# Performance work log

Measured on AMD Instinct MI355X. Metric: run time of the kernel, lower is better.

Reference implementation:

```python
import jax, jax.numpy as jnp
import numpy as np

N, E, IN, H, C, L = 50000, 800000, 256, 128, 50, 3
EPS = 1e-5  # BatchNorm1d eps


def setup_inputs() -> dict:
    key = jax.random.key(0)
    ks = jax.random.split(key, 16)
    s = 0.05  # weight init scale
    return dict(
        features=jax.random.normal(ks[0], (N, IN), jnp.float32),
        src=jax.random.randint(ks[1], (E,), 0, N, jnp.int32),
        dst=jax.random.randint(ks[2], (E,), 0, N, jnp.int32),
        w_in=jax.random.normal(ks[3], (IN, H), jnp.float32) * s,
        b_in=jnp.zeros((H,), jnp.float32),
        gc_w=jax.random.normal(ks[4], (L, H, H), jnp.float32) * s,
        gc_b=jnp.zeros((L, H), jnp.float32),
        bn_gamma=jnp.ones((L, H), jnp.float32),
        bn_beta=jnp.zeros((L, H), jnp.float32),
        bn_mean=jax.random.normal(ks[5], (L, H), jnp.float32) * 0.1,
        bn_var=jax.random.uniform(ks[6], (L, H), jnp.float32, 0.5, 1.5),
        attn_w1=jax.random.normal(ks[7], (2 * H, H), jnp.float32) * s,
        attn_b1=jnp.zeros((H,), jnp.float32),
        attn_w2=jax.random.normal(ks[8], (H, 1), jnp.float32) * s,
        attn_b2=jnp.zeros((1,), jnp.float32),
        agg_w=jax.random.normal(ks[9], (2 * H, H), jnp.float32) * s,
        agg_b=jnp.zeros((H,), jnp.float32),
        out_w=jax.random.normal(ks[10], (H, C), jnp.float32) * s,
        out_b=jnp.zeros((C,), jnp.float32),
    )


def reference(features, src, dst, w_in, b_in, gc_w, gc_b, bn_gamma, bn_beta,
              bn_mean, bn_var, attn_w1, attn_b1, attn_w2, attn_b2,
              agg_w, agg_b, out_w, out_b):
    seg = lambda v, i: jax.ops.segment_sum(v, i, num_segments=N)
    ones_e = jnp.ones((E,), features.dtype)
    in_deg = seg(ones_e, dst)    # [N] in-degree (dst side)
    out_deg = seg(ones_e, src)   # [N] out-degree (src side)

    # input_encoder (dropout = identity at inference)
    h = jax.nn.relu(features @ w_in + b_in)  # [N, H]

    # aggregate_neighbor_types: copy_u + mean (0 for zero in-degree)
    neigh = seg(h[src], dst) / jnp.maximum(in_deg, 1.0)[:, None]
    agg = jax.nn.relu(jnp.concatenate([h, neigh], axis=1) @ agg_w + agg_b)

    # relation attention: MLP -> sigmoid gate, gated residual add
    a = jax.nn.relu(jnp.concatenate([h, agg], axis=1) @ attn_w1 + attn_b1)
    attn = jax.nn.sigmoid(a @ attn_w2 + attn_b2)  # [N, 1]
    h_att = h + agg * attn

    # DGL GraphConv norm='both', clamp(min=1), aggregate-then-matmul
    inv_out = jnp.maximum(out_deg, 1.0)[:, None] ** -0.5
    inv_in = jnp.maximum(in_deg, 1.0)[:, None] ** -0.5
    for i in range(L):
        x = h_att if i == 0 else h
        rst = seg((x * inv_out)[src], dst) * inv_in  # normalized SpMM
        rst = rst @ gc_w[i] + gc_b[i]
        # BatchNorm1d (eval: running stats)
        rst = (rst - bn_mean[i]) * (bn_gamma[i] * jax.lax.rsqrt(bn_var[i] + EPS)) + bn_beta[i]
        rst = jax.nn.relu(rst)
        if i > 0:
            rst = rst + h  # residual
        h = rst

    return h @ out_w + out_b  # [N, C]
```

## Files before the change

### kernel.cpp

```cpp
#include <hip/hip_runtime.h>
#include <hip/hip_fp16.h>
#include <math.h>

constexpr int NN  = 50000;
constexpr int EE  = 800000;
constexpr int INF_ = 256;
constexpr int HF  = 128;
constexpr int CC  = 50;
constexpr long NH = (long)NN * HF;
constexpr int NSL = 32;
constexpr int ESL = EE / NSL;
constexpr int CHK = 12500;
#define EPSV 1e-5f

enum { EPI_RELU = 0, EPI_NONE = 1, EPI_BN = 2, EPI_BN_RES = 3, EPI_ATTN = 4 };
enum { H16_NONE = 0, H16_SCALED = 2 };

typedef __attribute__((ext_vector_type(4))) float f32x4;
typedef __attribute__((ext_vector_type(8))) _Float16 f16x8;


__global__ __launch_bounds__(256) void count_partial2_kernel(
    const int4* __restrict__ dst4, const int4* __restrict__ src4,
    unsigned* __restrict__ pd, unsigned* __restrict__ ps) {
  __shared__ unsigned cnt[CHK];
  int bb = blockIdx.x;
  const int which = bb >> 7;
  bb &= 127;
  const int4* keys4 = which ? src4 : dst4;
  unsigned* partials = which ? ps : pd;
  const int chunk = bb & 3;
  const int sl = bb >> 2;
  for (int i = threadIdx.x; i < CHK; i += 256) cnt[i] = 0;
  __syncthreads();
  const int base4 = sl * (ESL / 4);
  const int lo = chunk * CHK;
  for (int i = threadIdx.x; i < ESL / 4; i += 256) {
    int4 k = keys4[base4 + i];
    int a;
    a = k.x - lo; if ((unsigned)a < (unsigned)CHK) atomicAdd(&cnt[a], 1u);
    a = k.y - lo; if ((unsigned)a < (unsigned)CHK) atomicAdd(&cnt[a], 1u);
    a = k.z - lo; if ((unsigned)a < (unsigned)CHK) atomicAdd(&cnt[a], 1u);
    a = k.w - lo; if ((unsigned)a < (unsigned)CHK) atomicAdd(&cnt[a], 1u);
  }
  __syncthreads();
  unsigned* p = partials + (long)sl * NN + lo;
  for (int i = threadIdx.x; i < CHK; i += 256) p[i] = cnt[i];
}

__global__ __launch_bounds__(256) void deg_scan_kernel(
    const unsigned* __restrict__ pd, const unsigned* __restrict__ ps,
    int* __restrict__ row_ptr, int* __restrict__ bsum,
    float* __restrict__ inv_mean, float* __restrict__ inv_in,
    float* __restrict__ inv_out) {
  __shared__ int sh[256];
  int n = blockIdx.x * 256 + threadIdx.x;
  unsigned di = 0, dz = 0;
  if (n < NN) {
    #pragma unroll 8
    for (int sl = 0; sl < NSL; ++sl) {
      di += pd[(long)sl * NN + n];
      dz += ps[(long)sl * NN + n];
    }
    float fdi = fmaxf((float)di, 1.f), fdz = fmaxf((float)dz, 1.f);
    inv_mean[n] = 1.f / fdi;
    inv_in[n]  = rsqrtf(fdi);
    inv_out[n] = rsqrtf(fdz);
  }
  int v = (n < NN) ? (int)di : 0;
  sh[threadIdx.x] = v;
  __syncthreads();
  #pragma unroll
  for (int off = 1; off < 256; off <<= 1) {
    int tv = (threadIdx.x >= off) ? sh[threadIdx.x - off] : 0;
    __syncthreads();
    sh[threadIdx.x] += tv;
    __syncthreads();
  }
  if (n < NN) row_ptr[n] = sh[threadIdx.x] - v;
  if (threadIdx.x == 255) bsum[blockIdx.x] = sh[255];
}

__global__ __launch_bounds__(256) void scan_block_kernel(const int* __restrict__ counts,
                                                         int* excl, int* bsum, int n) {
  __shared__ int sh[256];
  int i = blockIdx.x * 256 + threadIdx.x;
  int v = (i < n) ? counts[i] : 0;
  sh[threadIdx.x] = v;
  __syncthreads();
  #pragma unroll
  for (int off = 1; off < 256; off <<= 1) {
    int tv = (threadIdx.x >= off) ? sh[threadIdx.x - off] : 0;
    __syncthreads();
    sh[threadIdx.x] += tv;
    __syncthreads();
  }
  if (i < n) excl[i] = sh[threadIdx.x] - v;
  if (threadIdx.x == 255 && bsum) bsum[blockIdx.x] = sh[255];
}

__global__ void cursor_init_kernel(const int* __restrict__ row_ptr, const int* __restrict__ bsum,
                                   const unsigned* __restrict__ pd,
                                   unsigned* __restrict__ cur0,
                                   const float* __restrict__ inv_mean,
                                   const float* __restrict__ inv_in,
                                   int4* __restrict__ nodeinfo) {
  int n = blockIdx.x * 256 + threadIdx.x;
  if (n >= NN) return;
  unsigned start = (unsigned)(row_ptr[n] + bsum[n >> 8]);
  unsigned run = start;
  #pragma unroll 8
  for (int sl = 0; sl < NSL; ++sl) {
    cur0[(long)sl * NN + n] = run;
    run += pd[(long)sl * NN + n];
  }
  nodeinfo[n] = make_int4((int)start, (int)run,
                          __float_as_int(inv_mean[n]), __float_as_int(inv_in[n]));
}

__global__ __launch_bounds__(256) void fill_partial_kernel(
    const int4* __restrict__ dst4, const int4* __restrict__ src4,
    const unsigned* __restrict__ cur0, int* __restrict__ col) {
  __shared__ unsigned cur[CHK];
  const int chunk = blockIdx.x & 3;
  const int sl = blockIdx.x >> 2;
  const int lo = chunk * CHK;
  const unsigned* c0 = cur0 + (long)sl * NN + lo;
  for (int i = threadIdx.x; i < CHK; i += 256) cur[i] = c0[i];
  __syncthreads();
  const int base4 = sl * (ESL / 4);
  for (int i = threadIdx.x; i < ESL / 4; i += 256) {
    int4 d = dst4[base4 + i];
    int4 s = src4[base4 + i];
    int a;
    a = d.x - lo; if ((unsigned)a < (unsigned)CHK) col[atomicAdd(&cur[a], 1u)] = s.x;
    a = d.y - lo; if ((unsigned)a < (unsigned)CHK) col[atomicAdd(&cur[a], 1u)] = s.y;
    a = d.z - lo; if ((unsigned)a < (unsigned)CHK) col[atomicAdd(&cur[a], 1u)] = s.z;
    a = d.w - lo; if ((unsigned)a < (unsigned)CHK) col[atomicAdd(&cur[a], 1u)] = s.w;
  }
}


__global__ __launch_bounds__(256) void spmm32p_kernel(
    const int4* __restrict__ nodeinfo, const int* __restrict__ cols,
    const __half* __restrict__ xs, int useW,
    __half* __restrict__ outh) {
  const int t = threadIdx.x;
  const int lane = t & 63;
  const int wv = t >> 6;
  const int b = blockIdx.x;
  const int xcd = b & 7;
  const int slice = xcd >> 1;
  const int sub = xcd & 1;
  const int npair = lane >> 5;
  const int node = (b >> 3) * 16 + sub * 8 + wv * 2 + npair;
  const int e8 = (lane >> 2) & 7;
  const int q4 = lane & 3;
  const __half* xb = xs + (long)slice * NN * 32 + q4 * 8;
  int4 ni = nodeinfo[node];
  const int e0 = ni.x, end = ni.y;
  const float d = __int_as_float(useW ? ni.w : ni.z);
  const int deg = end - e0;
  int dmax = deg > 0 ? deg : 0;
  {
    int od = __shfl_xor(dmax, 32, 64);
    dmax = dmax > od ? dmax : od;
  }
  const int kmax = (dmax + 7) >> 3;
  const int ecl = (end - 1) > 0 ? (end - 1) : 0;
  const __half2 z2 = __float2half2_rn(0.f);
  __half2 A0 = z2, A1 = z2, A2 = z2, A3 = z2;
  __half2 B0 = z2, B1 = z2, B2 = z2, B3 = z2;
  int k = 0;
  for (; k + 2 <= kmax; k += 2) {
    int ee0 = e0 + k * 8 + e8;
    int ee1 = ee0 + 8;
    bool m0 = ee0 < end, m1 = ee1 < end;
    int s0 = cols[m0 ? ee0 : ecl];
    int s1 = cols[m1 ? ee1 : ecl];
    f32x4 v0 = *(const f32x4*)(xb + (unsigned)s0 * 32u);
    f32x4 v1 = *(const f32x4*)(xb + (unsigned)s1 * 32u);
    const __half2* h0 = (const __half2*)&v0;
    const __half2* h1 = (const __half2*)&v1;
    A0 = __hadd2(A0, m0 ? h0[0] : z2); A1 = __hadd2(A1, m0 ? h0[1] : z2);
    A2 = __hadd2(A2, m0 ? h0[2] : z2); A3 = __hadd2(A3, m0 ? h0[3] : z2);
    B0 = __hadd2(B0, m1 ? h1[0] : z2); B1 = __hadd2(B1, m1 ? h1[1] : z2);
    B2 = __hadd2(B2, m1 ? h1[2] : z2); B3 = __hadd2(B3, m1 ? h1[3] : z2);
  }
  if (k < kmax) {
    int ee = e0 + k * 8 + e8;
    bool m = ee < end;
    int s = cols[m ? ee : ecl];
    f32x4 v = *(const f32x4*)(xb + (unsigned)s * 32u);
    const __half2* h = (const __half2*)&v;
    A0 = __hadd2(A0, m ? h[0] : z2); A1 = __hadd2(A1, m ? h[1] : z2);
    A2 = __hadd2(A2, m ? h[2] : z2); A3 = __hadd2(A3, m ? h[3] : z2);
  }
  A0 = __hadd2(A0, B0); A1 = __hadd2(A1, B1);
  A2 = __hadd2(A2, B2); A3 = __hadd2(A3, B3);
  float2 p0 = __half22float2(A0), p1 = __half22float2(A1);
  float2 p2 = __half22float2(A2), p3 = __half22float2(A3);
  float f0 = p0.x, f1 = p0.y, f2 = p1.x, f3 = p1.y;
  float f4 = p2.x, f5 = p2.y, f6 = p3.x, f7 = p3.y;
  {
    bool hi = (lane & 4) != 0;
    float t0 = hi ? f0 : f4, t1 = hi ? f1 : f5, t2 = hi ? f2 : f6, t3 = hi ? f3 : f7;
    t0 = __shfl_xor(t0, 4, 64); t1 = __shfl_xor(t1, 4, 64);
    t2 = __shfl_xor(t2, 4, 64); t3 = __shfl_xor(t3, 4, 64);
    f0 = (hi ? f4 : f0) + t0; f1 = (hi ? f5 : f1) + t1;
    f2 = (hi ? f6 : f2) + t2; f3 = (hi ? f7 : f3) + t3;
  }
  {
    bool hi = (lane & 8) != 0;
    float t0 = hi ? f0 : f2, t1 = hi ? f1 : f3;
    t0 = __shfl_xor(t0, 8, 64); t1 = __shfl_xor(t1, 8, 64);
    f0 = (hi ? f2 : f0) + t0; f1 = (hi ? f3 : f1) + t1;
  }
  float fin;
  {
    bool hi = (lane & 16) != 0;
    float t0 = hi ? f0 : f1;
    t0 = __shfl_xor(t0, 16, 64);
    fin = (hi ? f1 : f0) + t0;
  }
  int foff = q4 * 8 + ((lane >> 2) & 1) * 4 + ((lane >> 3) & 1) * 2 + ((lane >> 4) & 1);
  outh[((long)slice * NN + node) * 32 + foff] = __float2half(fin * d);
}


constexpr int SZ256 = 8 * 8 * 512;
constexpr int SZ128 = 4 * 8 * 512;
constexpr int SZOUT = 4 * 4 * 512;
constexpr int PK_TOTAL = 3 * SZ256 + 3 * SZ128 + SZOUT;

__global__ __launch_bounds__(256) void prepack_all_kernel(
    const float* __restrict__ w_in, const float* __restrict__ agg_w,
    const float* __restrict__ at1, const float* __restrict__ gc_w,
    const float* __restrict__ out_w, ushort* __restrict__ outbase) {
  int idx = blockIdx.x * 256 + threadIdx.x;
  if (idx >= PK_TOTAL) return;
  const float* W; int N, ldw, NTpad, local; ushort* outp;
  if (idx < 3 * SZ256) {
    int s = idx / SZ256; local = idx - s * SZ256;
    W = (s == 0) ? w_in : ((s == 1) ? agg_w : at1);
    N = HF; ldw = HF; NTpad = 8;
    outp = outbase + s * SZ256;
  } else if (idx < 3 * SZ256 + 3 * SZ128) {
    int r = idx - 3 * SZ256; int s = r / SZ128; local = r - s * SZ128;
    W = gc_w + (long)s * HF * HF; N = HF; ldw = HF; NTpad = 8;
    outp = outbase + 3 * SZ256 + s * SZ128;
  } else {
    local = idx - 3 * SZ256 - 3 * SZ128;
    W = out_w; N = CC; ldw = CC; NTpad = 4;
    outp = outbase + 3 * SZ256 + 3 * SZ128;
  }
  int j    = local & 7;
  int lane = (local >> 3) & 63;
  int rest = local >> 9;
  int nt = rest % NTpad;
  int kc = rest / NTpad;
  int k = kc * 32 + (lane >> 4) * 8 + j;
  int n = nt * 16 + (lane & 15);
  float w = (n < N) ? W[(long)k * ldw + n] : 0.f;
  outp[local] = __half_as_ushort(__float2half(w));
}


template<int KC, int NT, int NTP, int EPI, int H16, int ASRC, int OUTM, int COLSPLIT, int BHOIST>
__global__ __launch_bounds__(256) void mgemm_kernel(
    const void* __restrict__ A1, int lda1,
    const void* __restrict__ A2,
    const ushort* __restrict__ Bf,
    const float* __restrict__ bias,
    const float* __restrict__ g, const float* __restrict__ be,
    const float* __restrict__ mu, const float* __restrict__ va,
    const __half* __restrict__ resp,
    float* __restrict__ outf, __half* __restrict__ outh, int ldc, int Ncols,
    __half* __restrict__ x16, const float* __restrict__ rowscale) {
  const int t = threadIdx.x;
  const int lane = t & 63;
  const int wid = t >> 6;
  const int rowbase = COLSPLIT ? (blockIdx.x * 32 + (wid >> 1) * 16)
                               : (blockIdx.x * 64 + wid * 16);
  const int colbase = COLSPLIT ? ((wid & 1) * NT * 16) : 0;
  const int arow = rowbase + (lane & 15);
  const int kgrp = (lane >> 4) * 8;
  const bool rowok = arow < NN;

  f32x4 acc[NT];
  #pragma unroll
  for (int n = 0; n < NT; ++n) acc[n] = (f32x4){0.f, 0.f, 0.f, 0.f};

  const f32x4 z4 = {0.f, 0.f, 0.f, 0.f};
  f32x4 fra[ASRC == 0 ? KC : 1], frb[ASRC == 0 ? KC : 1];
  uint4 areg[ASRC == 1 ? KC : 1];
  if (ASRC == 0) {
    #pragma unroll
    for (int kc = 0; kc < KC; ++kc) {
      const float* p = (const float*)A1 + (long)arow * lda1 + kc * 32 + kgrp;
      fra[kc] = rowok ? *(const f32x4*)p : z4;
      frb[kc] = rowok ? *(const f32x4*)(p + 4) : z4;
    }
  } else {
    #pragma unroll
    for (int kc = 0; kc < KC; ++kc) {
      const bool second = (KC == 8) && (kc >= 4);
      const ushort* At = (const ushort*)(second ? A2 : A1);
      int k0 = (second ? (kc - 4) : kc) * 32 + kgrp;
      const ushort* p = At + ((long)(k0 >> 5) * NN + arow) * 32 + (k0 & 31);
      areg[kc] = rowok ? *(const uint4*)p : make_uint4(0, 0, 0, 0);
    }
  }

  if (BHOIST) {
    uint4 breg[KC * NT];
    #pragma unroll
    for (int kc = 0; kc < KC; ++kc) {
      const ushort* bp = Bf + ((long)kc * NTP * 64 + lane) * 8 + (long)colbase * 32;
      #pragma unroll
      for (int nt = 0; nt < NT; ++nt)
        breg[kc * NT + nt] = *(const uint4*)(bp + (long)nt * 512);
    }
    #pragma unroll
    for (int kc = 0; kc < KC; ++kc) {
      union { uint4 u; f16x8 v; } cv;
      cv.u = areg[kc];
      #pragma unroll
      for (int nt = 0; nt < NT; ++nt) {
        union { uint4 u; f16x8 v; } bv;
        bv.u = breg[kc * NT + nt];
        acc[nt] = __builtin_amdgcn_mfma_f32_16x16x32_f16(cv.v, bv.v, acc[nt], 0, 0, 0);
      }
    }
  } else {
    #pragma unroll
    for (int kc = 0; kc < KC; ++kc) {
      f16x8 av;
      if (ASRC == 0) {
        #pragma unroll
        for (int j = 0; j < 4; ++j) {
          av[j]     = (_Float16)fra[kc][j];
          av[j + 4] = (_Float16)frb[kc][j];
        }
      } else {
        union { uint4 u; f16x8 v; } cv;
        cv.u = areg[kc];
        av = cv.v;
      }
      const ushort* bp = Bf + ((long)kc * NTP * 64 + lane) * 8 + (long)colbase * 32;
      #pragma unroll
      for (int nt = 0; nt < NT; ++nt) {
        union { uint4 u; f16x8 v; } bv;
        bv.u = *(const uint4*)(bp + (long)nt * 512);
        acc[nt] = __builtin_amdgcn_mfma_f32_16x16x32_f16(av, bv.v, acc[nt], 0, 0, 0);
      }
    }
  }

  const int colg = lane & 15;
  const int rsub = (lane >> 4) * 4;

  if (EPI == EPI_ATTN) {
    float part0 = 0.f, part1 = 0.f, part2 = 0.f, part3 = 0.f;
    #pragma unroll
    for (int nt = 0; nt < NT; ++nt) {
      int c = nt * 16 + colg;
      float w2v = g[c];
      float bb = bias[c];
      part0 = fmaf(fmaxf(acc[nt][0] + bb, 0.f), w2v, part0);
      part1 = fmaf(fmaxf(acc[nt][1] + bb, 0.f), w2v, part1);
      part2 = fmaf(fmaxf(acc[nt][2] + bb, 0.f), w2v, part2);
      part3 = fmaf(fmaxf(acc[nt][3] + bb, 0.f), w2v, part3);
    }
    #pragma unroll
    for (int m = 1; m <= 8; m <<= 1) {
      part0 += __shfl_xor(part0, m, 64);
      part1 += __shfl_xor(part1, m, 64);
      part2 += __shfl_xor(part2, m, 64);
      part3 += __shfl_xor(part3, m, 64);
    }
    const float b2v = be[0];
    float s0 = 1.f / (1.f + __expf(-(part0 + b2v)));
    float s1 = 1.f / (1.f + __expf(-(part1 + b2v)));
    float s2 = 1.f / (1.f + __expf(-(part2 + b2v)));
    float s3 = 1.f / (1.f + __expf(-(part3 + b2v)));
    const __half* h0t = (const __half*)A1;
    const __half* aggt = (const __half*)A2;
    #pragma unroll
    for (int nt = 0; nt < NT; ++nt) {
      int c = nt * 16 + colg;
      #pragma unroll
      for (int i = 0; i < 4; ++i) {
        int r = rowbase + rsub + i;
        if (r >= NN) continue;
        long sidx = ((long)(c >> 5) * NN + r) * 32 + (c & 31);
        float sv = (i == 0) ? s0 : ((i == 1) ? s1 : ((i == 2) ? s2 : s3));
        float h = __half2float(h0t[sidx]) + __half2float(aggt[sidx]) * sv;
        x16[sidx] = __float2half(h * rowscale[r]);
      }
    }
    return;
  }

  #pragma unroll
  for (int nt = 0; nt < NT; ++nt) {
    int c = colbase + nt * 16 + colg;
    if (c >= Ncols) continue;
    float bb = bias ? bias[c] : 0.f;
    float scale = 1.f, shift = 0.f;
    if (EPI == EPI_BN || EPI == EPI_BN_RES) {
      scale = g[c] * rsqrtf(va[c] + EPSV);
      shift = be[c] - mu[c] * scale;
    }
    #pragma unroll
    for (int i = 0; i < 4; ++i) {
      int r = rowbase + rsub + i;
      if (r >= NN) continue;
      long sidx = ((long)(c >> 5) * NN + r) * 32 + (c & 31);
      float v = acc[nt][i] + bb;
      if (EPI == EPI_RELU) {
        v = fmaxf(v, 0.f);
      } else if (EPI == EPI_BN || EPI == EPI_BN_RES) {
        v = fmaxf(v * scale + shift, 0.f);
        if (EPI == EPI_BN_RES) v += __half2float(resp[sidx]);
      }
      if (OUTM == 0) {
        outf[(long)r * ldc + c] = v;
      } else {
        outh[sidx] = __float2half(v);
        if (H16 == H16_SCALED) x16[sidx] = __float2half(v * rowscale[r]);
      }
    }
  }
}


extern "C" void kernel_launch(void* const* d_in, const int* in_sizes, int n_in,
                              void* d_out, int out_size, void* d_ws, size_t ws_size,
                              hipStream_t stream) {
  const float* features = (const float*)d_in[0];
  const int*   src      = (const int*)d_in[1];
  const int*   dst      = (const int*)d_in[2];
  const float* w_in     = (const float*)d_in[3];
  const float* b_in     = (const float*)d_in[4];
  const float* gc_w     = (const float*)d_in[5];
  const float* gc_b     = (const float*)d_in[6];
  const float* bn_gamma = (const float*)d_in[7];
  const float* bn_beta  = (const float*)d_in[8];
  const float* bn_mean  = (const float*)d_in[9];
  const float* bn_var   = (const float*)d_in[10];
  const float* attn_w1  = (const float*)d_in[11];
  const float* attn_b1  = (const float*)d_in[12];
  const float* attn_w2  = (const float*)d_in[13];
  const float* attn_b2  = (const float*)d_in[14];
  const float* agg_w    = (const float*)d_in[15];
  const float* agg_b    = (const float*)d_in[16];
  const float* out_w    = (const float*)d_in[17];
  const float* out_b    = (const float*)d_in[18];
  float* out = (float*)d_out;

  float* fbase = (float*)d_ws;
  float* inv_mean = fbase;
  float* inv_in   = inv_mean + NN;
  float* inv_out  = inv_in + NN;
  int* row_ptr = (int*)(inv_out + NN);
  int* bsum    = row_ptr + NN + 16;
  int* col     = bsum + 256;
  int4* nodeinfo = (int4*)(col + EE);

  ushort* pk = (ushort*)(nodeinfo + NN);
  ushort* win_f = pk;
  ushort* agg_f = pk + SZ256;
  ushort* at1_f = pk + 2 * SZ256;
  ushort* gcf0  = pk + 3 * SZ256;
  ushort* gcf1  = gcf0 + SZ128;
  ushort* gcf2  = gcf1 + SZ128;
  ushort* ow_f  = gcf2 + SZ128;

  __half* T0 = (__half*)(ow_f + SZOUT);
  __half* T1 = T0 + NH;
  __half* T2 = T1 + NH;
  __half* X16 = T2 + NH;

  unsigned* pd   = (unsigned*)T0;
  unsigned* ps   = pd + (long)NSL * NN;
  unsigned* cur0 = ps + (long)NSL * NN;

  dim3 b256(256);
  const int gN = (NN + 255) / 256;
  const int gblocks = (NN + 63) / 64;
  const int gsplit  = (NN + 31) / 32;
  const int gspmm = (NN / 16) * 8;
  const int gpre = NSL * 4;

  count_partial2_kernel<<<2 * gpre, b256, 0, stream>>>(
      (const int4*)dst, (const int4*)src, pd, ps);
  deg_scan_kernel<<<gN, b256, 0, stream>>>(pd, ps, row_ptr, bsum, inv_mean, inv_in, inv_out);
  scan_block_kernel<<<1, b256, 0, stream>>>(bsum, bsum, nullptr, gN);
  cursor_init_kernel<<<gN, b256, 0, stream>>>(row_ptr, bsum, pd, cur0, inv_mean, inv_in, nodeinfo);
  fill_partial_kernel<<<gpre, b256, 0, stream>>>((const int4*)dst, (const int4*)src, cur0, col);

  prepack_all_kernel<<<(PK_TOTAL + 255) / 256, b256, 0, stream>>>(
      w_in, agg_w, attn_w1, gc_w, out_w, pk);

  mgemm_kernel<8, 4, 8, EPI_RELU, H16_NONE, 0, 1, 1, 0><<<gsplit, b256, 0, stream>>>(
      features, INF_, nullptr, win_f, b_in,
      nullptr, nullptr, nullptr, nullptr, nullptr,
      nullptr, T0, HF, HF, nullptr, nullptr);
  spmm32p_kernel<<<gspmm, b256, 0, stream>>>(nodeinfo, col, T0, 0, T1);
  mgemm_kernel<8, 4, 8, EPI_RELU, H16_NONE, 1, 1, 1, 0><<<gsplit, b256, 0, stream>>>(
      T0, 0, T1, agg_f, agg_b,
      nullptr, nullptr, nullptr, nullptr, nullptr,
      nullptr, T2, HF, HF, nullptr, nullptr);
  mgemm_kernel<8, 8, 8, EPI_ATTN, H16_NONE, 1, 1, 0, 0><<<gblocks, b256, 0, stream>>>(
      T0, 0, T2, at1_f, attn_b1,
      attn_w2, attn_b2, nullptr, nullptr, nullptr,
      nullptr, nullptr, HF, HF, X16, inv_out);

  spmm32p_kernel<<<gspmm, b256, 0, stream>>>(nodeinfo, col, X16, 1, T1);
  mgemm_kernel<4, 4, 8, EPI_BN, H16_SCALED, 1, 1, 1, 1><<<gsplit, b256, 0, stream>>>(
      T1, 0, nullptr, gcf0, gc_b,
      bn_gamma, bn_beta, bn_mean, bn_var, nullptr,
      nullptr, T2, HF, HF, X16, inv_out);
  spmm32p_kernel<<<gspmm, b256, 0, stream>>>(nodeinfo, col, X16, 1, T1);
  mgemm_kernel<4, 4, 8, EPI_BN_RES, H16_SCALED, 1, 1, 1, 1><<<gsplit, b256, 0, stream>>>(
      T1, 0, nullptr, gcf1, gc_b + HF,
      bn_gamma + HF, bn_beta + HF, bn_mean + HF, bn_var + HF, T2,
      nullptr, T0, HF, HF, X16, inv_out);
  spmm32p_kernel<<<gspmm, b256, 0, stream>>>(nodeinfo, col, X16, 1, T1);
  mgemm_kernel<4, 4, 8, EPI_BN_RES, H16_NONE, 1, 1, 1, 1><<<gsplit, b256, 0, stream>>>(
      T1, 0, nullptr, gcf2, gc_b + 2 * HF,
      bn_gamma + 2 * HF, bn_beta + 2 * HF, bn_mean + 2 * HF, bn_var + 2 * HF, T0,
      nullptr, T2, HF, HF, nullptr, nullptr);

  mgemm_kernel<4, 4, 4, EPI_NONE, H16_NONE, 1, 0, 0, 1><<<gblocks, b256, 0, stream>>>(
      T2, 0, nullptr, ow_f, out_b,
      nullptr, nullptr, nullptr, nullptr, nullptr,
      out, nullptr, CC, CC, nullptr, nullptr);
}
```

Measured before the change: 319.8 us.

## Merge preprocessing and input GEMM launches into fused multi-role kernels

```diff
diff --git a/kernel.cpp b/kernel.cpp
--- a/kernel.cpp
+++ b/kernel.cpp
@@ -19,95 +19,185 @@
 typedef __attribute__((ext_vector_type(4))) float f32x4;
 typedef __attribute__((ext_vector_type(8))) _Float16 f16x8;
 
-
-__global__ __launch_bounds__(256) void count_partial2_kernel(
+constexpr int SZ256 = 8 * 8 * 512;
+constexpr int SZ128 = 4 * 8 * 512;
+constexpr int SZOUT = 4 * 4 * 512;
+constexpr int PK_TOTAL = 3 * SZ256 + 3 * SZ128 + SZOUT;
+constexpr int PKB = (PK_TOTAL + 255) / 256;
+
+
+__global__ __launch_bounds__(256) void fuse1_kernel(
     const int4* __restrict__ dst4, const int4* __restrict__ src4,
-    unsigned* __restrict__ pd, unsigned* __restrict__ ps) {
+    unsigned* __restrict__ pd, unsigned* __restrict__ ps,
+    const float* __restrict__ w_in, const float* __restrict__ agg_w,
+    const float* __restrict__ at1, const float* __restrict__ gc_w,
+    const float* __restrict__ out_w, ushort* __restrict__ outbase) {
   __shared__ unsigned cnt[CHK];
-  int bb = blockIdx.x;
-  const int which = bb >> 7;
-  bb &= 127;
-  const int4* keys4 = which ? src4 : dst4;
-  unsigned* partials = which ? ps : pd;
-  const int chunk = bb & 3;
-  const int sl = bb >> 2;
-  for (int i = threadIdx.x; i < CHK; i += 256) cnt[i] = 0;
-  __syncthreads();
-  const int base4 = sl * (ESL / 4);
-  const int lo = chunk * CHK;
-  for (int i = threadIdx.x; i < ESL / 4; i += 256) {
-    int4 k = keys4[base4 + i];
-    int a;
-    a = k.x - lo; if ((unsigned)a < (unsigned)CHK) atomicAdd(&cnt[a], 1u);
-    a = k.y - lo; if ((unsigned)a < (unsigned)CHK) atomicAdd(&cnt[a], 1u);
-    a = k.z - lo; if ((unsigned)a < (unsigned)CHK) atomicAdd(&cnt[a], 1u);
-    a = k.w - lo; if ((unsigned)a < (unsigned)CHK) atomicAdd(&cnt[a], 1u);
-  }
-  __syncthreads();
-  unsigned* p = partials + (long)sl * NN + lo;
-  for (int i = threadIdx.x; i < CHK; i += 256) p[i] = cnt[i];
-}
-
-__global__ __launch_bounds__(256) void deg_scan_kernel(
+  if (blockIdx.x < 256) {
+    int bb = blockIdx.x;
+    const int which = bb >> 7;
+    bb &= 127;
+    const int4* keys4 = which ? src4 : dst4;
+    unsigned* partials = which ? ps : pd;
+    const int chunk = bb & 3;
+    const int sl = bb >> 2;
+    for (int i = threadIdx.x; i < CHK; i += 256) cnt[i] = 0;
+    __syncthreads();
+    const int base4 = sl * (ESL / 4);
+    const int lo = chunk * CHK;
+    for (int i = threadIdx.x; i < ESL / 4; i += 256) {
+      int4 k = keys4[base4 + i];
+      int a;
+      a = k.x - lo; if ((unsigned)a < (unsigned)CHK) atomicAdd(&cnt[a], 1u);
+      a = k.y - lo; if ((unsigned)a < (unsigned)CHK) atomicAdd(&cnt[a], 1u);
+      a = k.z - lo; if ((unsigned)a < (unsigned)CHK) atomicAdd(&cnt[a], 1u);
+      a = k.w - lo; if ((unsigned)a < (unsigned)CHK) atomicAdd(&cnt[a], 1u);
+    }
+    __syncthreads();
+    unsigned* p = partials + (long)sl * NN + lo;
+    for (int i = threadIdx.x; i < CHK; i += 256) p[i] = cnt[i];
+    return;
+  }
+  int idx = (blockIdx.x - 256) * 256 + threadIdx.x;
+  if (idx >= PK_TOTAL) return;
+  const float* W; int N, ldw, NTpad, local; ushort* outp;
+  if (idx < 3 * SZ256) {
+    int s = idx / SZ256; local = idx - s * SZ256;
+    W = (s == 0) ? w_in : ((s == 1) ? agg_w : at1);
+    N = HF; ldw = HF; NTpad = 8;
+    outp = outbase + s * SZ256;
+  } else if (idx < 3 * SZ256 + 3 * SZ128) {
+    int r = idx - 3 * SZ256; int s = r / SZ128; local = r - s * SZ128;
+    W = gc_w + (long)s * HF * HF; N = HF; ldw = HF; NTpad = 8;
+    outp = outbase + 3 * SZ256 + s * SZ128;
+  } else {
+    local = idx - 3 * SZ256 - 3 * SZ128;
+    W = out_w; N = CC; ldw = CC; NTpad = 4;
+    outp = outbase + 3 * SZ256 + 3 * SZ128;
+  }
+  int j    = local & 7;
+  int lane = (local >> 3) & 63;
+  int rest = local >> 9;
+  int nt = rest % NTpad;
+  int kc = rest / NTpad;
+  int k = kc * 32 + (lane >> 4) * 8 + j;
+  int n = nt * 16 + (lane & 15);
+  float w = (n < N) ? W[(long)k * ldw + n] : 0.f;
+  outp[local] = __half_as_ushort(__float2half(w));
+}
+
+
+constexpr int GSPLIT = (NN + 31) / 32;
+constexpr int GN = (NN + 255) / 256;
+
+__global__ __launch_bounds__(256) void fuse2_kernel(
+    const float* __restrict__ features, const ushort* __restrict__ Bf,
+    const float* __restrict__ bias, __half* __restrict__ outh,
     const unsigned* __restrict__ pd, const unsigned* __restrict__ ps,
     int* __restrict__ row_ptr, int* __restrict__ bsum,
     float* __restrict__ inv_mean, float* __restrict__ inv_in,
     float* __restrict__ inv_out) {
   __shared__ int sh[256];
-  int n = blockIdx.x * 256 + threadIdx.x;
-  unsigned di = 0, dz = 0;
-  if (n < NN) {
-    #pragma unroll 8
-    for (int sl = 0; sl < NSL; ++sl) {
-      di += pd[(long)sl * NN + n];
-      dz += ps[(long)sl * NN + n];
-    }
-    float fdi = fmaxf((float)di, 1.f), fdz = fmaxf((float)dz, 1.f);
-    inv_mean[n] = 1.f / fdi;
-    inv_in[n]  = rsqrtf(fdi);
-    inv_out[n] = rsqrtf(fdz);
-  }
-  int v = (n < NN) ? (int)di : 0;
-  sh[threadIdx.x] = v;
+  if (blockIdx.x >= GSPLIT) {
+    int n = (blockIdx.x - GSPLIT) * 256 + threadIdx.x;
+    unsigned di = 0, dz = 0;
+    if (n < NN) {
+      #pragma unroll 8
+      for (int sl = 0; sl < NSL; ++sl) {
+        di += pd[(long)sl * NN + n];
+        dz += ps[(long)sl * NN + n];
+      }
+      float fdi = fmaxf((float)di, 1.f), fdz = fmaxf((float)dz, 1.f);
+      inv_mean[n] = 1.f / fdi;
+      inv_in[n]  = rsqrtf(fdi);
+      inv_out[n] = rsqrtf(fdz);
+    }
+    int v = (n < NN) ? (int)di : 0;
+    sh[threadIdx.x] = v;
+    __syncthreads();
+    #pragma unroll
+    for (int off = 1; off < 256; off <<= 1) {
+      int tv = (threadIdx.x >= off) ? sh[threadIdx.x - off] : 0;
+      __syncthreads();
+      sh[threadIdx.x] += tv;
+      __syncthreads();
+    }
+    if (n < NN) row_ptr[n] = sh[threadIdx.x] - v;
+    if (threadIdx.x == 255) bsum[blockIdx.x - GSPLIT] = sh[255];
+    return;
+  }
+  const int t = threadIdx.x;
+  const int lane = t & 63;
+  const int wid = t >> 6;
+  const int rowbase = blockIdx.x * 32 + (wid >> 1) * 16;
+  const int colbase = (wid & 1) * 64;
+  const int arow = rowbase + (lane & 15);
+  const int kgrp = (lane >> 4) * 8;
+  const bool rowok = arow < NN;
+
+  f32x4 acc[4];
+  #pragma unroll
+  for (int n = 0; n < 4; ++n) acc[n] = (f32x4){0.f, 0.f, 0.f, 0.f};
+  const f32x4 z4 = {0.f, 0.f, 0.f, 0.f};
+  f32x4 fra[8], frb[8];
+  #pragma unroll
+  for (int kc = 0; kc < 8; ++kc) {
+    const float* p = features + (long)arow * INF_ + kc * 32 + kgrp;
+    fra[kc] = rowok ? *(const f32x4*)p : z4;
+    frb[kc] = rowok ? *(const f32x4*)(p + 4) : z4;
+  }
+  #pragma unroll
+  for (int kc = 0; kc < 8; ++kc) {
+    f16x8 av;
+    #pragma unroll
+    for (int j = 0; j < 4; ++j) {
+      av[j]     = (_Float16)fra[kc][j];
+      av[j + 4] = (_Float16)frb[kc][j];
+    }
+    const ushort* bp = Bf + ((long)kc * 8 * 64 + lane) * 8 + (long)colbase * 32;
+    #pragma unroll
+    for (int nt = 0; nt < 4; ++nt) {
+      union { uint4 u; f16x8 v; } bv;
+      bv.u = *(const uint4*)(bp + (long)nt * 512);
+      acc[nt] = __builtin_amdgcn_mfma_f32_16x16x32_f16(av, bv.v, acc[nt], 0, 0, 0);
+    }
+  }
+  const int colg = lane & 15;
+  const int rsub = (lane >> 4) * 4;
+  #pragma unroll
+  for (int nt = 0; nt < 4; ++nt) {
+    int c = colbase + nt * 16 + colg;
+    float bb = bias[c];
+    #pragma unroll
+    for (int i = 0; i < 4; ++i) {
+      int r = rowbase + rsub + i;
+      if (r >= NN) continue;
+      long sidx = ((long)(c >> 5) * NN + r) * 32 + (c & 31);
+      outh[sidx] = __float2half(fmaxf(acc[nt][i] + bb, 0.f));
+    }
+  }
+}
+
+
+__global__ __launch_bounds__(256) void cursor_init2_kernel(
+    const int* __restrict__ row_ptr, const int* __restrict__ bsum,
+    const unsigned* __restrict__ pd, unsigned* __restrict__ cur0,
+    const float* __restrict__ inv_mean, const float* __restrict__ inv_in,
+    int4* __restrict__ nodeinfo) {
+  __shared__ int sh[256];
+  int part = 0;
+  for (int j = threadIdx.x; j < (int)blockIdx.x; j += 256) part += bsum[j];
+  sh[threadIdx.x] = part;
   __syncthreads();
   #pragma unroll
-  for (int off = 1; off < 256; off <<= 1) {
-    int tv = (threadIdx.x >= off) ? sh[threadIdx.x - off] : 0;
+  for (int off = 128; off >= 1; off >>= 1) {
+    if (threadIdx.x < off) sh[threadIdx.x] += sh[threadIdx.x + off];
     __syncthreads();
-    sh[threadIdx.x] += tv;
-    __syncthreads();
-  }
-  if (n < NN) row_ptr[n] = sh[threadIdx.x] - v;
-  if (threadIdx.x == 255) bsum[blockIdx.x] = sh[255];
-}
-
-__global__ __launch_bounds__(256) void scan_block_kernel(const int* __restrict__ counts,
-                                                         int* excl, int* bsum, int n) {
-  __shared__ int sh[256];
-  int i = blockIdx.x * 256 + threadIdx.x;
-  int v = (i < n) ? counts[i] : 0;
-  sh[threadIdx.x] = v;
-  __syncthreads();
-  #pragma unroll
-  for (int off = 1; off < 256; off <<= 1) {
-    int tv = (threadIdx.x >= off) ? sh[threadIdx.x - off] : 0;
-    __syncthreads();
-    sh[threadIdx.x] += tv;
-    __syncthreads();
-  }
-  if (i < n) excl[i] = sh[threadIdx.x] - v;
-  if (threadIdx.x == 255 && bsum) bsum[blockIdx.x] = sh[255];
-}
-
-__global__ void cursor_init_kernel(const int* __restrict__ row_ptr, const int* __restrict__ bsum,
-                                   const unsigned* __restrict__ pd,
-                                   unsigned* __restrict__ cur0,
-                                   const float* __restrict__ inv_mean,
-                                   const float* __restrict__ inv_in,
-                                   int4* __restrict__ nodeinfo) {
+  }
+  const int boff = sh[0];
   int n = blockIdx.x * 256 + threadIdx.x;
   if (n >= NN) return;
-  unsigned start = (unsigned)(row_ptr[n] + bsum[n >> 8]);
+  unsigned start = (unsigned)(row_ptr[n] + boff);
   unsigned run = start;
   #pragma unroll 8
   for (int sl = 0; sl < NSL; ++sl) {
@@ -228,44 +318,6 @@
 }
 
 
-constexpr int SZ256 = 8 * 8 * 512;
-constexpr int SZ128 = 4 * 8 * 512;
-constexpr int SZOUT = 4 * 4 * 512;
-constexpr int PK_TOTAL = 3 * SZ256 + 3 * SZ128 + SZOUT;
-
-__global__ __launch_bounds__(256) void prepack_all_kernel(
-    const float* __restrict__ w_in, const float* __restrict__ agg_w,
-    const float* __restrict__ at1, const float* __restrict__ gc_w,
-    const float* __restrict__ out_w, ushort* __restrict__ outbase) {
-  int idx = blockIdx.x * 256 + threadIdx.x;
-  if (idx >= PK_TOTAL) return;
-  const float* W; int N, ldw, NTpad, local; ushort* outp;
-  if (idx < 3 * SZ256) {
-    int s = idx / SZ256; local = idx - s * SZ256;
-    W = (s == 0) ? w_in : ((s == 1) ? agg_w : at1);
-    N = HF; ldw = HF; NTpad = 8;
-    outp = outbase + s * SZ256;
-  } else if (idx < 3 * SZ256 + 3 * SZ128) {
-    int r = idx - 3 * SZ256; int s = r / SZ128; local = r - s * SZ128;
-    W = gc_w + (long)s * HF * HF; N = HF; ldw = HF; NTpad = 8;
-    outp = outbase + 3 * SZ256 + s * SZ128;
-  } else {
-    local = idx - 3 * SZ256 - 3 * SZ128;
-    W = out_w; N = CC; ldw = CC; NTpad = 4;
-    outp = outbase + 3 * SZ256 + 3 * SZ128;
-  }
-  int j    = local & 7;
-  int lane = (local >> 3) & 63;
-  int rest = local >> 9;
-  int nt = rest % NTpad;
-  int kc = rest / NTpad;
-  int k = kc * 32 + (lane >> 4) * 8 + j;
-  int n = nt * 16 + (lane & 15);
-  float w = (n < N) ? W[(long)k * ldw + n] : 0.f;
-  outp[local] = __half_as_ushort(__float2half(w));
-}
-
-
 template<int KC, int NT, int NTP, int EPI, int H16, int ASRC, int OUTM, int COLSPLIT, int BHOIST>
 __global__ __launch_bounds__(256) void mgemm_kernel(
     const void* __restrict__ A1, int lda1,
@@ -482,31 +534,28 @@
   __half* T2 = T1 + NH;
   __half* X16 = T2 + NH;
 
-  unsigned* pd   = (unsigned*)T0;
+  unsigned* pd   = (unsigned*)T1;
   unsigned* ps   = pd + (long)NSL * NN;
-  unsigned* cur0 = ps + (long)NSL * NN;
+  unsigned* cur0 = (unsigned*)T2;
 
   dim3 b256(256);
-  const int gN = (NN + 255) / 256;
   const int gblocks = (NN + 63) / 64;
-  const int gsplit  = (NN + 31) / 32;
+  const int gsplit  = GSPLIT;
   const int gspmm = (NN / 16) * 8;
   const int gpre = NSL * 4;
 
-  count_partial2_kernel<<<2 * gpre, b256, 0, stream>>>(
-      (const int4*)dst, (const int4*)src, pd, ps);
-  deg_scan_kernel<<<gN, b256, 0, stream>>>(pd, ps, row_ptr, bsum, inv_mean, inv_in, inv_out);
-  scan_block_kernel<<<1, b256, 0, stream>>>(bsum, bsum, nullptr, gN);
-  cursor_init_kernel<<<gN, b256, 0, stream>>>(row_ptr, bsum, pd, cur0, inv_mean, inv_in, nodeinfo);
+  fuse1_kernel<<<256 + PKB, b256, 0, stream>>>(
+      (const int4*)dst, (const int4*)src, pd, ps,
+      w_in, agg_w, attn_w1, gc_w, out_w, pk);
+
+  fuse2_kernel<<<GSPLIT + GN, b256, 0, stream>>>(
+      features, win_f, b_in, T0,
+      pd, ps, row_ptr, bsum, inv_mean, inv_in, inv_out);
+
+  cursor_init2_kernel<<<GN, b256, 0, stream>>>(
+      row_ptr, bsum, pd, cur0, inv_mean, inv_in, nodeinfo);
   fill_partial_kernel<<<gpre, b256, 0, stream>>>((const int4*)dst, (const int4*)src, cur0, col);
 
-  prepack_all_kernel<<<(PK_TOTAL + 255) / 256, b256, 0, stream>>>(
-      w_in, agg_w, attn_w1, gc_w, out_w, pk);
-
-  mgemm_kernel<8, 4, 8, EPI_RELU, H16_NONE, 0, 1, 1, 0><<<gsplit, b256, 0, stream>>>(
-      features, INF_, nullptr, win_f, b_in,
-      nullptr, nullptr, nullptr, nullptr, nullptr,
-      nullptr, T0, HF, HF, nullptr, nullptr);
   spmm32p_kernel<<<gspmm, b256, 0, stream>>>(nodeinfo, col, T0, 0, T1);
   mgemm_kernel<8, 4, 8, EPI_RELU, H16_NONE, 1, 1, 1, 0><<<gsplit, b256, 0, stream>>>(
       T0, 0, T1, agg_f, agg_b,
```

After: 310.5 us. -2.9%, faster.
